# Kernel optimization log

Hardware: AMD Instinct MI355X
Metric: run time of the kernel (lower is better)

The kernel has to match this reference:

```python
import jax, jax.numpy as jnp
import numpy as np

B, N, T, C = 16, 12, 128, 128  # batch, num_classes (nodes), temporal, channels


def _bn(x, gamma, beta, eps=1e-5):
    # BatchNorm2d in training mode: stats over (batch, t, c), channel axis 1, biased var
    mean = jnp.mean(x, axis=(0, 2, 3), keepdims=True)
    var = jnp.var(x, axis=(0, 2, 3), keepdims=True)
    xn = (x - mean) * jax.lax.rsqrt(var + eps)
    return xn * gamma[None, :, None, None] + beta[None, :, None, None]


def setup_inputs() -> dict:
    key = jax.random.key(0)
    ks = jax.random.split(key, 3)
    scale = np.float32(np.sqrt(2.0 / C))
    inp = {
        'x': jax.random.normal(ks[0], (B, N, T, C), dtype=jnp.float32),
        'edge': jax.random.normal(ks[1], (B, N * N, T, C), dtype=jnp.float32),
    }
    wk = jax.random.split(ks[2], 10)
    for name, k in zip(['A1', 'B1', 'E1', 'U1', 'V1', 'A2', 'B2', 'E2', 'U2', 'V2'], wk):
        inp[name] = jax.random.normal(k, (C, C), dtype=jnp.float32) * scale
    for name, dim in [('g_e1', N * N), ('b_e1', N * N), ('g_v1', N), ('b_v1', N),
                      ('g_e2', N * N), ('b_e2', N * N), ('g_v2', N), ('b_v2', N)]:
        inp[name] = jnp.ones((dim,), jnp.float32) if name[0] == 'g' else jnp.zeros((dim,), jnp.float32)
    return inp


def _forward(x, edge, A1, B1, E1, U1, V1, A2, B2, E2, U2, V2,
             g_e1, b_e1, g_v1, b_v1, g_e2, b_e2, g_v2, b_v2):
    # create_e_matrix: edge index e = i*N + j; 'end' selects node i, 'start' selects node j.
    # Dense incidence einsums become pure gathers; the transpose einsum is a
    # scatter-add over j, i.e. a reshape + sum.
    i_idx = jnp.repeat(jnp.arange(N), N)  # end-node of each edge
    j_idx = jnp.tile(jnp.arange(N), N)    # start-node of each edge
    b, _, t, c = x.shape

    def layer(x, edge, A, Bw, E, U, V, ge, be, gv, bv, mask_node):
        res = x
        edge_upd = (x @ A.T)[:, i_idx] + (x @ Bw.T)[:, j_idx] + edge @ E.T
        edge_upd = _bn(edge_upd, ge, be)
        edge_upd = jnp.where(jnp.isnan(edge_upd), 0.0, edge_upd)
        edge = edge + jax.nn.relu(edge_upd)
        e = jax.nn.sigmoid(edge)
        e = jax.nn.softmax(e.reshape(b, N, N, t, c), axis=2).reshape(b, N * N, t, c)
        Ujx = (x @ V.T)[:, j_idx]
        agg = (e * Ujx).reshape(b, N, N, t, c).sum(axis=2) / N  # scatter to end nodes
        xn = _bn(x @ U.T + agg, gv, bv)
        if mask_node:  # original only NaN-masks node BN in layer 1
            xn = jnp.where(jnp.isnan(xn), 0.0, xn)
        return jax.nn.relu(res + xn), edge

    x, edge = layer(x, edge, A1, B1, E1, U1, V1, g_e1, b_e1, g_v1, b_v1, True)
    x, edge = layer(x, edge, A2, B2, E2, U2, V2, g_e2, b_e2, g_v2, b_v2, False)
    return x, edge


def reference(x, edge, A1, B1, E1, U1, V1, A2, B2, E2, U2, V2,
              g_e1, b_e1, g_v1, b_v1, g_e2, b_e2, g_v2, b_v2):
    return _forward(x, edge, A1, B1, E1, U1, V1, A2, B2, E2, U2, V2,
                    g_e1, b_e1, g_v1, b_v1, g_e2, b_e2, g_v2, b_v2)
```

## Files before the change

### kernel.cpp

```cpp
#include <hip/hip_runtime.h>
#include <hip/hip_bf16.h>

#define BB 16
#define NN 12
#define NE 144
#define TT 128
#define CC 128

typedef __attribute__((ext_vector_type(8))) short v8s;
typedef __attribute__((ext_vector_type(4))) short v4s;
typedef __attribute__((ext_vector_type(4))) float v4f;

__device__ __forceinline__ short f2bf(float f) {
    unsigned u = __float_as_uint(f);
    u += 0x7fffu + ((u >> 16) & 1u);
    return (short)(u >> 16);
}
__device__ __forceinline__ float bf2f(unsigned short u) {
    return __uint_as_float(((unsigned)u) << 16);
}
__device__ __forceinline__ v4s f4_to_bf4(float4 a) {
    v4s r; r[0] = f2bf(a.x); r[1] = f2bf(a.y); r[2] = f2bf(a.z); r[3] = f2bf(a.w); return r;
}

__global__ __launch_bounds__(256) void kW(
    const float* A1, const float* B1, const float* E1, const float* U1, const float* V1,
    const float* A2, const float* B2, const float* E2, const float* U2, const float* V2,
    unsigned short* wb)
{
    int idx = blockIdx.x * 256 + threadIdx.x;
    int w = idx >> 14, r = idx & 16383;
    const float* s;
    switch (w) {
        case 0: s = A1; break; case 1: s = B1; break; case 2: s = E1; break;
        case 3: s = U1; break; case 4: s = V1; break; case 5: s = A2; break;
        case 6: s = B2; break; case 7: s = E2; break; case 8: s = U2; break;
        default: s = V2; break;
    }
    wb[idx] = (unsigned short)f2bf(s[r]);
}

__global__ __launch_bounds__(256) void kP(
    const float* __restrict__ x, const unsigned short* __restrict__ wb,
    int sA, int sB, int sV, int sU,
    unsigned short* __restrict__ oA, unsigned short* __restrict__ oB,
    unsigned short* __restrict__ oV, unsigned short* __restrict__ oU)
{
    __shared__ unsigned short xt[64][136];
    int tid = threadIdx.x;
    int m0 = blockIdx.x * 64;
    #pragma unroll
    for (int it = 0; it < 8; ++it) {
        int f = it * 256 + tid;
        int row = f >> 5, c4 = f & 31;
        float4 v = *reinterpret_cast<const float4*>(x + (size_t)m0 * 128 + (size_t)f * 4);
        *reinterpret_cast<v4s*>(&xt[row][c4 * 4]) = f4_to_bf4(v);
    }
    __syncthreads();
    int lane = tid & 63, wid = tid >> 6;
    int l15 = lane & 15, l4 = lane >> 4;

    const unsigned short* Ws[4] = { wb + (size_t)sA * 16384, wb + (size_t)sB * 16384,
                                    wb + (size_t)sV * 16384, wb + (size_t)sU * 16384 };
    unsigned short* Os[4] = { oA, oB, oV, oU };

    #pragma unroll
    for (int w = 0; w < 4; ++w) {
        const unsigned short* W = Ws[w];
        unsigned short* out = Os[w];
        v8s bfr[2][4];
        #pragma unroll
        for (int nt2 = 0; nt2 < 2; ++nt2) {
            int col = (wid * 2 + nt2) * 16 + l15;
            #pragma unroll
            for (int kk = 0; kk < 4; ++kk)
                bfr[nt2][kk] = *reinterpret_cast<const v8s*>(W + col * 128 + kk * 32 + l4 * 8);
        }
        v4f acc[4][2] = {};
        #pragma unroll
        for (int kk = 0; kk < 4; ++kk) {
            #pragma unroll
            for (int mt = 0; mt < 4; ++mt) {
                v8s a = *reinterpret_cast<const v8s*>(&xt[mt * 16 + l15][kk * 32 + l4 * 8]);
                acc[mt][0] = __builtin_amdgcn_mfma_f32_16x16x32_bf16(a, bfr[0][kk], acc[mt][0], 0, 0, 0);
                acc[mt][1] = __builtin_amdgcn_mfma_f32_16x16x32_bf16(a, bfr[1][kk], acc[mt][1], 0, 0, 0);
            }
        }
        #pragma unroll
        for (int mt = 0; mt < 4; ++mt) {
            #pragma unroll
            for (int nt2 = 0; nt2 < 2; ++nt2) {
                int col = (wid * 2 + nt2) * 16 + l15;
                #pragma unroll
                for (int reg = 0; reg < 4; ++reg) {
                    int rowg = m0 + mt * 16 + l4 * 4 + reg;
                    out[(size_t)rowg * 128 + col] = (unsigned short)f2bf(acc[mt][nt2][reg]);
                }
            }
        }
    }
}

template<bool IN_F32>
__global__ __launch_bounds__(256, 4) void kA(
    const float* __restrict__ ef32, const unsigned short* __restrict__ ebf_in,
    unsigned short* __restrict__ ebf_out,
    unsigned short* __restrict__ updg,
    const unsigned short* __restrict__ xAp, const unsigned short* __restrict__ xBp,
    const unsigned short* __restrict__ Ebf, float2* __restrict__ epart)
{
    __shared__ unsigned short et[64][136];
    __shared__ float sblk[2];
    int tid = threadIdx.x;
    int bid = blockIdx.x;
    int th = bid & 1; int m = bid >> 1;
    int e = m % NE, b = m / NE;
    int iA = e / 12, jA = e - iA * 12;
    int t0 = th * 64;
    if (tid < 2) sblk[tid] = 0.f;
    size_t erow0 = ((size_t)(b * NE + e) * TT + t0) * CC;

    if constexpr (IN_F32) {
        #pragma unroll
        for (int it = 0; it < 8; ++it) {
            int f = it * 256 + tid;
            int row = f >> 5, c4 = f & 31;
            float4 v = *reinterpret_cast<const float4*>(ef32 + erow0 + (size_t)row * CC + c4 * 4);
            v4s bv = f4_to_bf4(v);
            *reinterpret_cast<v4s*>(&et[row][c4 * 4]) = bv;
            *reinterpret_cast<v4s*>(ebf_out + erow0 + (size_t)row * CC + c4 * 4) = bv;
        }
    } else {
        #pragma unroll
        for (int it = 0; it < 4; ++it) {
            int f = it * 256 + tid;
            int row = f >> 4, c8 = f & 15;
            *reinterpret_cast<v8s*>(&et[row][c8 * 8]) =
                *reinterpret_cast<const v8s*>(ebf_in + erow0 + (size_t)row * CC + c8 * 8);
        }
    }
    __syncthreads();

    int lane = tid & 63, wid = tid >> 6;
    int l15 = lane & 15, l4 = lane >> 4;

    v8s bfr[2][4];
    #pragma unroll
    for (int nt2 = 0; nt2 < 2; ++nt2) {
        int col = (wid * 2 + nt2) * 16 + l15;
        #pragma unroll
        for (int kk = 0; kk < 4; ++kk)
            bfr[nt2][kk] = *reinterpret_cast<const v8s*>(Ebf + col * 128 + kk * 32 + l4 * 8);
    }
    v4f acc[4][2] = {};
    #pragma unroll
    for (int kk = 0; kk < 4; ++kk) {
        #pragma unroll
        for (int mt = 0; mt < 4; ++mt) {
            v8s a = *reinterpret_cast<const v8s*>(&et[mt * 16 + l15][kk * 32 + l4 * 8]);
            acc[mt][0] = __builtin_amdgcn_mfma_f32_16x16x32_bf16(a, bfr[0][kk], acc[mt][0], 0, 0, 0);
            acc[mt][1] = __builtin_amdgcn_mfma_f32_16x16x32_bf16(a, bfr[1][kk], acc[mt][1], 0, 0, 0);
        }
    }
    __syncthreads();
    #pragma unroll
    for (int mt = 0; mt < 4; ++mt) {
        #pragma unroll
        for (int nt2 = 0; nt2 < 2; ++nt2) {
            int col = (wid * 2 + nt2) * 16 + l15;
            #pragma unroll
            for (int reg = 0; reg < 4; ++reg)
                et[mt * 16 + l4 * 4 + reg][col] = (unsigned short)f2bf(acc[mt][nt2][reg]);
        }
    }
    __syncthreads();
    size_t xaoff = ((size_t)(b * NN + iA) * TT + t0) * CC;
    size_t xboff = ((size_t)(b * NN + jA) * TT + t0) * CC;
    float s = 0.f, q = 0.f;
    #pragma unroll
    for (int it = 0; it < 4; ++it) {
        int f = it * 256 + tid;
        int row = f >> 4, c8 = f & 15;
        v8s ev = *reinterpret_cast<const v8s*>(&et[row][c8 * 8]);
        v8s xa = *reinterpret_cast<const v8s*>(xAp + xaoff + (size_t)row * CC + c8 * 8);
        v8s xb = *reinterpret_cast<const v8s*>(xBp + xboff + (size_t)row * CC + c8 * 8);
        v8s outv;
        #pragma unroll
        for (int k = 0; k < 8; ++k) {
            float v = bf2f((unsigned short)ev[k]) + bf2f((unsigned short)xa[k])
                    + bf2f((unsigned short)xb[k]);
            s += v; q += v * v;
            outv[k] = f2bf(v);
        }
        *reinterpret_cast<v8s*>(updg + erow0 + (size_t)row * CC + c8 * 8) = outv;
    }
    #pragma unroll
    for (int off = 1; off < 64; off <<= 1) { s += __shfl_xor(s, off); q += __shfl_xor(q, off); }
    if (lane == 0) { atomicAdd(&sblk[0], s); atomicAdd(&sblk[1], q); }
    __syncthreads();
    if (tid == 0) epart[bid] = make_float2(sblk[0], sblk[1]);
}

__global__ __launch_bounds__(64) void kRede(
    const float2* __restrict__ epart, const float* __restrict__ g,
    const float* __restrict__ be, float* __restrict__ estats)
{
    int e = blockIdx.x;
    int tid = threadIdx.x;
    float s = 0.f, q = 0.f;
    if (tid < 32) {
        int b = tid >> 1, th = tid & 1;
        float2 p = epart[(size_t)(b * NE + e) * 2 + th];
        s = p.x; q = p.y;
    }
    #pragma unroll
    for (int off = 1; off < 32; off <<= 1) { s += __shfl_xor(s, off); q += __shfl_xor(q, off); }
    if (tid == 0) {
        const float M = 262144.f;
        float mean = s / M;
        float var = q / M - mean * mean;
        float sc = g[e] * rsqrtf(var + 1e-5f);
        estats[e * 2] = sc;
        estats[e * 2 + 1] = be[e] - mean * sc;
    }
}

template<bool OUT_F32>
__global__ __launch_bounds__(256) void kC(
    unsigned short* __restrict__ ebf,
    float* __restrict__ eout,
    const unsigned short* __restrict__ updg,
    const unsigned short* __restrict__ xV, const unsigned short* __restrict__ xU,
    const float* __restrict__ estats,
    unsigned short* __restrict__ yout, float* __restrict__ npart)
{
    __shared__ unsigned short rb[48][136];
    __shared__ unsigned short xv[12][136];
    __shared__ float2 scf[48];
    __shared__ float ns[4], nq[4];
    int tid = threadIdx.x;
    int bid = blockIdx.x;
    int third = bid % 3; int bt = bid / 3;
    int b = bt >> 7, t = bt & 127;
    if (tid < 48) scf[tid] = make_float2(estats[(third * 48 + tid) * 2],
                                         estats[(third * 48 + tid) * 2 + 1]);
    if (tid < 4) { ns[tid] = 0.f; nq[tid] = 0.f; }
    if (tid < 192) {
        int row = tid >> 4, c8 = tid & 15;
        *reinterpret_cast<v8s*>(&xv[row][c8 * 8]) =
            *reinterpret_cast<const v8s*>(xV + (((size_t)(b * NN + row) * TT) + t) * CC + c8 * 8);
    }
    __syncthreads();
    int lane = tid & 63;
    #pragma unroll
    for (int it = 0; it < 3; ++it) {
        int f = it * 256 + tid;
        int row = f >> 4, c8 = f & 15;
        int eg = third * 48 + row;
        size_t goff = (((size_t)(b * NE + eg) * TT) + t) * CC + c8 * 8;
        v8s uv = *reinterpret_cast<const v8s*>(updg + goff);
        v8s ev = *reinterpret_cast<const v8s*>(ebf + goff);
        float2 sc = scf[row];
        float en[8]; v8s nv;
        #pragma unroll
        for (int k = 0; k < 8; ++k) {
            float bn = fmaxf(sc.x * bf2f((unsigned short)uv[k]) + sc.y, 0.f);
            en[k] = bf2f((unsigned short)ev[k]) + bn;
            nv[k] = f2bf(en[k]);
        }
        *reinterpret_cast<v8s*>(&rb[row][c8 * 8]) = nv;
        if constexpr (OUT_F32) {
            *reinterpret_cast<float4*>(eout + goff)     = make_float4(en[0], en[1], en[2], en[3]);
            *reinterpret_cast<float4*>(eout + goff + 4) = make_float4(en[4], en[5], en[6], en[7]);
        } else {
            *reinterpret_cast<v8s*>(ebf + goff) = nv;
        }
    }
    __syncthreads();
    #pragma unroll
    for (int ph = 0; ph < 2; ++ph) {
        int u = tid + ph * 256;
        int il = u >> 7, c = u & 127;
        float den = 0.f, ag = 0.f;
        #pragma unroll
        for (int j = 0; j < 12; ++j) {
            float sv = bf2f(rb[il * 12 + j][c]);
            float sg = 1.f / (1.f + __expf(-sv));
            float ev = __expf(sg);
            den += ev;
            ag += ev * bf2f(xv[j][c]);
        }
        float agg = ag / (den * 12.f);
        int i = third * 4 + il;
        size_t xa = (((size_t)(b * NN + i) * TT) + t) * CC + c;
        float yv = bf2f(xU[xa]) + agg;
        unsigned short us = (unsigned short)f2bf(yv);
        yout[xa] = us;
        float yr = bf2f(us);
        float s1 = yr, s2 = yr * yr;
        #pragma unroll
        for (int off = 1; off < 64; off <<= 1) { s1 += __shfl_xor(s1, off); s2 += __shfl_xor(s2, off); }
        if (lane == 0) { atomicAdd(&ns[il], s1); atomicAdd(&nq[il], s2); }
    }
    __syncthreads();
    if (tid < 4) {
        npart[(size_t)bid * 8 + tid * 2 + 0] = ns[tid];
        npart[(size_t)bid * 8 + tid * 2 + 1] = nq[tid];
    }
}

__global__ __launch_bounds__(256) void kRedn(
    const float* __restrict__ npart, const float* __restrict__ g,
    const float* __restrict__ be, float* __restrict__ nstats)
{
    int n = blockIdx.x;
    int third = n >> 2, il = n & 3;
    float s = 0.f, q = 0.f;
    for (int bt = threadIdx.x; bt < 2048; bt += 256) {
        const float* p = npart + ((size_t)(bt * 3 + third) * 8 + il * 2);
        s += p[0]; q += p[1];
    }
    __shared__ float ss[4], qq[4];
    #pragma unroll
    for (int off = 32; off >= 1; off >>= 1) { s += __shfl_down(s, off); q += __shfl_down(q, off); }
    int wid = threadIdx.x >> 6;
    if ((threadIdx.x & 63) == 0) { ss[wid] = s; qq[wid] = q; }
    __syncthreads();
    if (threadIdx.x == 0) {
        s = ss[0] + ss[1] + ss[2] + ss[3];
        q = qq[0] + qq[1] + qq[2] + qq[3];
        const float M = 262144.f;
        float mean = s / M;
        float var = q / M - mean * mean;
        float sc = g[n] * rsqrtf(var + 1e-5f);
        nstats[n * 2] = sc;
        nstats[n * 2 + 1] = be[n] - mean * sc;
    }
}

__global__ __launch_bounds__(256) void kE(
    const float* xres, const unsigned short* __restrict__ yin,
    const float* __restrict__ nstats, float* xout)
{
    int idx4 = blockIdx.x * 256 + threadIdx.x;
    size_t base = (size_t)idx4 * 4;
    int n = (int)((base >> 14) % 12);
    float scv = nstats[n * 2], shv = nstats[n * 2 + 1];
    float4 xvv = *reinterpret_cast<const float4*>(xres + base);
    v4s yv4 = *reinterpret_cast<const v4s*>(yin + base);
    float4 o;
    o.x = fmaxf(xvv.x + scv * bf2f((unsigned short)yv4[0]) + shv, 0.f);
    o.y = fmaxf(xvv.y + scv * bf2f((unsigned short)yv4[1]) + shv, 0.f);
    o.z = fmaxf(xvv.z + scv * bf2f((unsigned short)yv4[2]) + shv, 0.f);
    o.w = fmaxf(xvv.w + scv * bf2f((unsigned short)yv4[3]) + shv, 0.f);
    *reinterpret_cast<float4*>(xout + base) = o;
}

extern "C" void kernel_launch(void* const* d_in, const int* in_sizes, int n_in,
                              void* d_out, int out_size, void* d_ws, size_t ws_size,
                              hipStream_t stream)
{
    const float* x0 = (const float*)d_in[0];
    const float* e0 = (const float*)d_in[1];
    const float* W[10];
    for (int i = 0; i < 10; ++i) W[i] = (const float*)d_in[2 + i];
    const float* ge1 = (const float*)d_in[12];
    const float* be1 = (const float*)d_in[13];
    const float* gv1 = (const float*)d_in[14];
    const float* bv1 = (const float*)d_in[15];
    const float* ge2 = (const float*)d_in[16];
    const float* be2 = (const float*)d_in[17];
    const float* gv2 = (const float*)d_in[18];
    const float* bv2 = (const float*)d_in[19];

    const size_t SZX = (size_t)BB * NN * TT * CC;
    const size_t SZE = (size_t)BB * NE * TT * CC;
    float* out_x = (float*)d_out;
    float* out_e = out_x + SZX;

    unsigned short* ws16 = (unsigned short*)d_ws;
    unsigned short* xA = ws16;
    unsigned short* xB = ws16 + SZX;
    unsigned short* xV = ws16 + 2 * SZX;
    unsigned short* xU = ws16 + 3 * SZX;
    unsigned short* yb = ws16 + 4 * SZX;
    unsigned short* ebf = ws16 + 5 * SZX;
    unsigned short* upd = ebf + SZE;
    float2* epart  = (float2*)(upd + SZE);
    float* estats = (float*)(epart + 4608);
    float* npart  = estats + 288;
    float* nstats = npart + 49152;
    unsigned short* wb = (unsigned short*)(nstats + 24);

    float* x1 = out_x;

    kW<<<640, 256, 0, stream>>>(W[0], W[1], W[2], W[3], W[4], W[5], W[6], W[7], W[8], W[9], wb);

    kP<<<384, 256, 0, stream>>>(x0, wb, 0, 1, 4, 3, xA, xB, xV, xU);
    kA<true><<<4608, 256, 0, stream>>>(e0, nullptr, ebf, upd, xA, xB, wb + 2 * 16384, epart);
    kRede<<<144, 64, 0, stream>>>(epart, ge1, be1, estats);
    kC<false><<<6144, 256, 0, stream>>>(ebf, nullptr, upd, xV, xU, estats, yb, npart);
    kRedn<<<12, 256, 0, stream>>>(npart, gv1, bv1, nstats);
    kE<<<3072, 256, 0, stream>>>(x0, yb, nstats, x1);

    kP<<<384, 256, 0, stream>>>(x1, wb, 5, 6, 9, 8, xA, xB, xV, xU);
    kA<false><<<4608, 256, 0, stream>>>(nullptr, ebf, nullptr, upd, xA, xB, wb + 7 * 16384, epart);
    kRede<<<144, 64, 0, stream>>>(epart, ge2, be2, estats);
    kC<true><<<6144, 256, 0, stream>>>(ebf, out_e, upd, xV, xU, estats, yb, npart);
    kRedn<<<12, 256, 0, stream>>>(npart, gv2, bv2, nstats);
    kE<<<3072, 256, 0, stream>>>(x1, yb, nstats, out_x);
}
```

Before: 285.2 us.

## Recompute edge update GEMM in kC instead of storing intermediate to global

Kernel kA no longer writes the bf16 edge-update tensor and only produces BN partial statistics. Kernel kC now loads the edge tile into shared memory and recomputes edge@E^T with MFMA. It adds the gathered xA/xB rows, then applies BN, ReLU and the residual in place. This removes a full edge-sized global write and read per layer in exchange for doing the GEMM twice. It also sets a launch bound of 4 blocks per SM for kC and drops the upd workspace buffer.

```diff
diff --git a/kernel.cpp b/kernel.cpp
--- a/kernel.cpp
+++ b/kernel.cpp
@@ -19,6 +19,7 @@
 __device__ __forceinline__ float bf2f(unsigned short u) {
     return __uint_as_float(((unsigned)u) << 16);
 }
+__device__ __forceinline__ float rndbf(float f) { return bf2f((unsigned short)f2bf(f)); }
 __device__ __forceinline__ v4s f4_to_bf4(float4 a) {
     v4s r; r[0] = f2bf(a.x); r[1] = f2bf(a.y); r[2] = f2bf(a.z); r[3] = f2bf(a.w); return r;
 }
@@ -105,7 +106,6 @@
 __global__ __launch_bounds__(256, 4) void kA(
     const float* __restrict__ ef32, const unsigned short* __restrict__ ebf_in,
     unsigned short* __restrict__ ebf_out,
-    unsigned short* __restrict__ updg,
     const unsigned short* __restrict__ xAp, const unsigned short* __restrict__ xBp,
     const unsigned short* __restrict__ Ebf, float2* __restrict__ epart)
 {
@@ -184,15 +184,12 @@
         v8s ev = *reinterpret_cast<const v8s*>(&et[row][c8 * 8]);
         v8s xa = *reinterpret_cast<const v8s*>(xAp + xaoff + (size_t)row * CC + c8 * 8);
         v8s xb = *reinterpret_cast<const v8s*>(xBp + xboff + (size_t)row * CC + c8 * 8);
-        v8s outv;
         #pragma unroll
         for (int k = 0; k < 8; ++k) {
             float v = bf2f((unsigned short)ev[k]) + bf2f((unsigned short)xa[k])
                     + bf2f((unsigned short)xb[k]);
             s += v; q += v * v;
-            outv[k] = f2bf(v);
-        }
-        *reinterpret_cast<v8s*>(updg + erow0 + (size_t)row * CC + c8 * 8) = outv;
+        }
     }
     #pragma unroll
     for (int off = 1; off < 64; off <<= 1) { s += __shfl_xor(s, off); q += __shfl_xor(q, off); }
@@ -226,15 +223,16 @@
 }
 
 template<bool OUT_F32>
-__global__ __launch_bounds__(256) void kC(
+__global__ __launch_bounds__(256, 4) void kC(
     unsigned short* __restrict__ ebf,
     float* __restrict__ eout,
-    const unsigned short* __restrict__ updg,
+    const unsigned short* __restrict__ xAp, const unsigned short* __restrict__ xBp,
     const unsigned short* __restrict__ xV, const unsigned short* __restrict__ xU,
-    const float* __restrict__ estats,
+    const unsigned short* __restrict__ Ebf, const float* __restrict__ estats,
     unsigned short* __restrict__ yout, float* __restrict__ npart)
 {
-    __shared__ unsigned short rb[48][136];
+    __shared__ unsigned short et[48][136];
+    __shared__ unsigned short xab[16][136];
     __shared__ unsigned short xv[12][136];
     __shared__ float2 scf[48];
     __shared__ float ns[4], nq[4];
@@ -245,38 +243,79 @@
     if (tid < 48) scf[tid] = make_float2(estats[(third * 48 + tid) * 2],
                                          estats[(third * 48 + tid) * 2 + 1]);
     if (tid < 4) { ns[tid] = 0.f; nq[tid] = 0.f; }
+    {
+        int row = tid >> 4, c8 = tid & 15;
+        const unsigned short* src = (row < 4)
+            ? (xAp + (((size_t)(b * NN + third * 4 + row) * TT) + t) * CC)
+            : (xBp + (((size_t)(b * NN + (row - 4)) * TT) + t) * CC);
+        *reinterpret_cast<v8s*>(&xab[row][c8 * 8]) = *reinterpret_cast<const v8s*>(src + c8 * 8);
+    }
     if (tid < 192) {
         int row = tid >> 4, c8 = tid & 15;
         *reinterpret_cast<v8s*>(&xv[row][c8 * 8]) =
             *reinterpret_cast<const v8s*>(xV + (((size_t)(b * NN + row) * TT) + t) * CC + c8 * 8);
     }
-    __syncthreads();
-    int lane = tid & 63;
     #pragma unroll
     for (int it = 0; it < 3; ++it) {
         int f = it * 256 + tid;
         int row = f >> 4, c8 = f & 15;
-        int eg = third * 48 + row;
-        size_t goff = (((size_t)(b * NE + eg) * TT) + t) * CC + c8 * 8;
-        v8s uv = *reinterpret_cast<const v8s*>(updg + goff);
-        v8s ev = *reinterpret_cast<const v8s*>(ebf + goff);
-        float2 sc = scf[row];
-        float en[8]; v8s nv;
-        #pragma unroll
-        for (int k = 0; k < 8; ++k) {
-            float bn = fmaxf(sc.x * bf2f((unsigned short)uv[k]) + sc.y, 0.f);
-            en[k] = bf2f((unsigned short)ev[k]) + bn;
-            nv[k] = f2bf(en[k]);
-        }
-        *reinterpret_cast<v8s*>(&rb[row][c8 * 8]) = nv;
-        if constexpr (OUT_F32) {
-            *reinterpret_cast<float4*>(eout + goff)     = make_float4(en[0], en[1], en[2], en[3]);
-            *reinterpret_cast<float4*>(eout + goff + 4) = make_float4(en[4], en[5], en[6], en[7]);
-        } else {
-            *reinterpret_cast<v8s*>(ebf + goff) = nv;
-        }
-    }
-    __syncthreads();
+        *reinterpret_cast<v8s*>(&et[row][c8 * 8]) =
+            *reinterpret_cast<const v8s*>(ebf + (((size_t)(b * NE + third * 48 + row) * TT) + t) * CC + c8 * 8);
+    }
+    __syncthreads();
+    int lane = tid & 63, wid = tid >> 6;
+    int l15 = lane & 15, l4 = lane >> 4;
+
+    v8s bfr[2][4];
+    #pragma unroll
+    for (int nt2 = 0; nt2 < 2; ++nt2) {
+        int col = (wid * 2 + nt2) * 16 + l15;
+        #pragma unroll
+        for (int kk = 0; kk < 4; ++kk)
+            bfr[nt2][kk] = *reinterpret_cast<const v8s*>(Ebf + col * 128 + kk * 32 + l4 * 8);
+    }
+    v4f acc[3][2] = {};
+    #pragma unroll
+    for (int kk = 0; kk < 4; ++kk) {
+        #pragma unroll
+        for (int mt = 0; mt < 3; ++mt) {
+            v8s a = *reinterpret_cast<const v8s*>(&et[mt * 16 + l15][kk * 32 + l4 * 8]);
+            acc[mt][0] = __builtin_amdgcn_mfma_f32_16x16x32_bf16(a, bfr[0][kk], acc[mt][0], 0, 0, 0);
+            acc[mt][1] = __builtin_amdgcn_mfma_f32_16x16x32_bf16(a, bfr[1][kk], acc[mt][1], 0, 0, 0);
+        }
+    }
+    __syncthreads();
+    #pragma unroll
+    for (int mt = 0; mt < 3; ++mt) {
+        #pragma unroll
+        for (int reg = 0; reg < 4; ++reg) {
+            int r = mt * 16 + l4 * 4 + reg;
+            int il = r / 12, jl = r - il * 12;
+            float2 sc = scf[r];
+            #pragma unroll
+            for (int nt2 = 0; nt2 < 2; ++nt2) {
+                int col = (wid * 2 + nt2) * 16 + l15;
+                float upd = rndbf(acc[mt][nt2][reg]) + bf2f(xab[il][col]) + bf2f(xab[4 + jl][col]);
+                float bn = fmaxf(sc.x * upd + sc.y, 0.f);
+                float en = bf2f(et[r][col]) + bn;
+                et[r][col] = (unsigned short)f2bf(en);
+                if constexpr (OUT_F32) {
+                    int eg = third * 48 + r;
+                    eout[(((size_t)(b * NE + eg) * TT) + t) * CC + col] = en;
+                }
+            }
+        }
+    }
+    __syncthreads();
+    if constexpr (!OUT_F32) {
+        #pragma unroll
+        for (int it = 0; it < 3; ++it) {
+            int f = it * 256 + tid;
+            int row = f >> 4, c8 = f & 15;
+            *reinterpret_cast<v8s*>(ebf + (((size_t)(b * NE + third * 48 + row) * TT) + t) * CC + c8 * 8) =
+                *reinterpret_cast<const v8s*>(&et[row][c8 * 8]);
+        }
+    }
     #pragma unroll
     for (int ph = 0; ph < 2; ++ph) {
         int u = tid + ph * 256;
@@ -284,7 +323,7 @@
         float den = 0.f, ag = 0.f;
         #pragma unroll
         for (int j = 0; j < 12; ++j) {
-            float sv = bf2f(rb[il * 12 + j][c]);
+            float sv = bf2f(et[il * 12 + j][c]);
             float sg = 1.f / (1.f + __expf(-sv));
             float ev = __expf(sg);
             den += ev;
@@ -385,8 +424,7 @@
     unsigned short* xU = ws16 + 3 * SZX;
     unsigned short* yb = ws16 + 4 * SZX;
     unsigned short* ebf = ws16 + 5 * SZX;
-    unsigned short* upd = ebf + SZE;
-    float2* epart  = (float2*)(upd + SZE);
+    float2* epart  = (float2*)(ebf + SZE);
     float* estats = (float*)(epart + 4608);
     float* npart  = estats + 288;
     float* nstats = npart + 49152;
@@ -397,16 +435,18 @@
     kW<<<640, 256, 0, stream>>>(W[0], W[1], W[2], W[3], W[4], W[5], W[6], W[7], W[8], W[9], wb);
 
     kP<<<384, 256, 0, stream>>>(x0, wb, 0, 1, 4, 3, xA, xB, xV, xU);
-    kA<true><<<4608, 256, 0, stream>>>(e0, nullptr, ebf, upd, xA, xB, wb + 2 * 16384, epart);
+    kA<true><<<4608, 256, 0, stream>>>(e0, nullptr, ebf, xA, xB, wb + 2 * 16384, epart);
     kRede<<<144, 64, 0, stream>>>(epart, ge1, be1, estats);
-    kC<false><<<6144, 256, 0, stream>>>(ebf, nullptr, upd, xV, xU, estats, yb, npart);
+    kC<false><<<6144, 256, 0, stream>>>(ebf, nullptr, xA, xB, xV, xU,
+                                        wb + 2 * 16384, estats, yb, npart);
     kRedn<<<12, 256, 0, stream>>>(npart, gv1, bv1, nstats);
     kE<<<3072, 256, 0, stream>>>(x0, yb, nstats, x1);
 
     kP<<<384, 256, 0, stream>>>(x1, wb, 5, 6, 9, 8, xA, xB, xV, xU);
-    kA<false><<<4608, 256, 0, stream>>>(nullptr, ebf, nullptr, upd, xA, xB, wb + 7 * 16384, epart);
+    kA<false><<<4608, 256, 0, stream>>>(nullptr, ebf, nullptr, xA, xB, wb + 7 * 16384, epart);
     kRede<<<144, 64, 0, stream>>>(epart, ge2, be2, estats);
-    kC<true><<<6144, 256, 0, stream>>>(ebf, out_e, upd, xV, xU, estats, yb, npart);
+    kC<true><<<6144, 256, 0, stream>>>(ebf, out_e, xA, xB, xV, xU,
+                                       wb + 7 * 16384, estats, yb, npart);
     kRedn<<<12, 256, 0, stream>>>(npart, gv2, bv2, nstats);
     kE<<<3072, 256, 0, stream>>>(x1, yb, nstats, out_x);
 }
```

New measurement: 274.9 us. 3.6% less time.
